# Kernel tuning notes

Measured on AMD Instinct MI355X. Metric: run time of the kernel, lower is better.

The kernel has to match this reference:

```python
import jax, jax.numpy as jnp
import numpy as np

N_NODES = 50000
N_EDGES = 600000
D = 128
EDGE_DIM = 1
N_LAYERS = 2
NEG_SLOPE = 0.2


def setup_inputs() -> dict:
    key = jax.random.key(0)
    ks = jax.random.split(key, 8)
    x = jax.random.normal(ks[0], (N_NODES, D), dtype=jnp.float32)
    edge_index = jax.random.randint(ks[1], (2, N_EDGES), 0, N_NODES, dtype=jnp.int64)
    edge_attr = jax.random.normal(ks[2], (N_EDGES, EDGE_DIM), dtype=jnp.float32)
    s = 1.0 / np.sqrt(D)
    Wl = jax.random.normal(ks[3], (N_LAYERS, D, D), dtype=jnp.float32) * s   # lin_l weights
    Wr = jax.random.normal(ks[4], (N_LAYERS, D, D), dtype=jnp.float32) * s   # lin_r weights
    We = jax.random.normal(ks[5], (N_LAYERS, EDGE_DIM, D), dtype=jnp.float32) * s  # lin_edge
    att = jax.random.normal(ks[6], (N_LAYERS, D), dtype=jnp.float32) * s     # attention vector (heads=1)
    bias = jnp.zeros((N_LAYERS, D), dtype=jnp.float32)
    return {"x": x, "edge_index": edge_index, "edge_attr": edge_attr,
            "Wl": Wl, "Wr": Wr, "We": We, "att": att, "bias": bias}


def _gatv2_layer(x, src, dst, edge_attr, Wl, Wr, We, att, bias):
    # GATv2Conv, heads=1, add_self_loops=False, share_weights=False.
    xl = x @ Wl                                   # [N, D] (source transform)
    xr = x @ Wr                                   # [N, D] (target transform)
    m = xl[src] + xr[dst] + edge_attr @ We        # [E, D]
    m = jax.nn.leaky_relu(m, NEG_SLOPE)
    logits = m @ att                              # [E]
    # segment softmax over incoming edges of each dst node
    mx = jax.ops.segment_max(logits, dst, num_segments=N_NODES)  # [N]
    ex = jnp.exp(logits - mx[dst])                # [E]
    denom = jax.ops.segment_sum(ex, dst, num_segments=N_NODES)   # [N]
    alpha = ex / jnp.maximum(denom[dst], 1e-16)   # [E]
    out = jax.ops.segment_sum(alpha[:, None] * xl[src], dst, num_segments=N_NODES)
    return out + bias


def reference(x, edge_index, edge_attr, Wl, Wr, We, att, bias):
    src, dst = edge_index[0], edge_index[1]
    h = x
    for l in range(N_LAYERS):
        h = _gatv2_layer(h, src, dst, edge_attr, Wl[l], Wr[l], We[l], att[l], bias[l])
        h = jax.nn.relu(h)   # activation; norm=None, dropout=0 (eval) are identity
    return h
```

## Files before the change

kernel.cpp:

```cpp
#include <hip/hip_runtime.h>
#include <hip/hip_fp16.h>

#define N_NODES 50000
#define N_PAD   50048
#define N_EDGES 600000
#define DD 128
#define NEG_SLOPE 0.2f
#define BSHIFT 7
#define NBUCKETS 391
#define MAXB 2048
#define GGRID (N_PAD / 64)

typedef _Float16 h2 __attribute__((ext_vector_type(2)));
typedef _Float16 h8 __attribute__((ext_vector_type(8)));
typedef __attribute__((ext_vector_type(4))) float f32x4;
typedef unsigned long long u64;

__device__ inline h2 bch2(unsigned u) { return __builtin_bit_cast(h2, u); }
__device__ inline unsigned h2u(h2 h) { return __builtin_bit_cast(unsigned, h); }
__device__ inline ushort f2h_bits(float x) {
    return __builtin_bit_cast(ushort, (_Float16)x);
}

#if __has_builtin(__builtin_amdgcn_fdot2)
#define DOT2(a, b, c) __builtin_amdgcn_fdot2((a), (b), (c), false)
#else
#define DOT2(a, b, c) ((c) + (float)(a)[0] * (float)(b)[0] + (float)(a)[1] * (float)(b)[1])
#endif

__global__ void pack_detect(const float* __restrict__ Wl, const float* __restrict__ Wr,
                            ushort* __restrict__ Wp,
                            const int* __restrict__ ei, int* __restrict__ flag,
                            int* __restrict__ bcount) {
    if (blockIdx.x == 256) {
        for (int t = threadIdx.x; t < NBUCKETS; t += 256) bcount[t] = 0;
        if (threadIdx.x == 0) {
            int is64 = 1;
            for (int i = 0; i < 64; ++i) {
                if (ei[2 * i + 1] != 0) { is64 = 0; break; }
            }
            *flag = is64;
        }
        return;
    }
    int idx = blockIdx.x * 256 + threadIdx.x;
    int layer = idx >> 15;
    int which = (idx >> 14) & 1;
    int kk    = (idx >> 12) & 3;
    int c     = (idx >> 9) & 7;
    int lane  = (idx >> 3) & 63;
    int j     = idx & 7;
    int k   = kk * 32 + (lane >> 4) * 8 + j;
    int col = c * 16 + (lane & 15);
    const float* W = which ? Wr : Wl;
    Wp[idx] = f2h_bits(W[(size_t)layer * DD * DD + k * DD + col]);
}

__global__ __launch_bounds__(512) void bin_edges(
    const int* __restrict__ ei, const int* __restrict__ flag,
    const float* __restrict__ ea, int* __restrict__ bcount,
    u64* __restrict__ tmp) {
    __shared__ int lhist[NBUCKETS];
    __shared__ int lbase[NBUCKETS];
    for (int i = threadIdx.x; i < NBUCKETS; i += 512) lhist[i] = 0;
    __syncthreads();
    const bool is64 = (*flag) != 0;
    int base = blockIdx.x * 4096;
    int myb[8], myrank[8];
    u64 mypack[8];
    #pragma unroll
    for (int i = 0; i < 8; ++i) {
        int e = base + i * 512 + threadIdx.x;
        if (e < N_EDGES) {
            int s, d;
            if (is64) {
                const long long* e64 = (const long long*)ei;
                s = (int)e64[e];
                d = (int)e64[N_EDGES + e];
            } else {
                s = ei[e];
                d = ei[N_EDGES + e];
            }
            unsigned hb = (unsigned)f2h_bits(ea[e]);
            int b = d >> BSHIFT;
            myb[i] = b;
            mypack[i] = ((u64)(unsigned)(d & 127) << 32) | ((u64)hb << 16) | (unsigned)s;
            myrank[i] = atomicAdd(&lhist[b], 1);
        } else myb[i] = -1;
    }
    __syncthreads();
    for (int i = threadIdx.x; i < NBUCKETS; i += 512) {
        int c = lhist[i];
        lbase[i] = c ? atomicAdd(&bcount[i], c) : 0;
    }
    __syncthreads();
    #pragma unroll
    for (int i = 0; i < 8; ++i)
        if (myb[i] >= 0) {
            int rel = lbase[myb[i]] + myrank[i];
            if (rel < MAXB)
                tmp[(size_t)myb[i] * MAXB + rel] = mypack[i];
        }
}

__global__ __launch_bounds__(256) void scatter_gemm(
    const u64* __restrict__ tmp, const int* __restrict__ bcount,
    unsigned* __restrict__ se_csr, int* __restrict__ row_start,
    const float* __restrict__ xf, const ushort* __restrict__ Wp,
    ushort* __restrict__ xl, ushort* __restrict__ xr) {
    __shared__ ushort wlds[32768];
    int tid = threadIdx.x;

    if (blockIdx.x < NBUCKETS) {
        int* bscan = (int*)wlds;
        int* lcnt  = (int*)wlds + 512;
        int* lscan = (int*)wlds + 640;
        int* lcur  = (int*)wlds + 768;
        {
            int v = 0;
            if (tid < NBUCKETS) { v = bcount[tid]; if (v > MAXB) v = MAXB; }
            bscan[tid] = v;
            int v2 = 0;
            if (tid + 256 < NBUCKETS) { v2 = bcount[tid + 256]; if (v2 > MAXB) v2 = MAXB; }
            bscan[tid + 256] = v2;
        }
        __syncthreads();
        #pragma unroll
        for (int off = 1; off < 512; off <<= 1) {
            int t0 = (tid >= off) ? bscan[tid - off] : 0;
            int t1 = (tid + 256 >= off) ? bscan[tid + 256 - off] : 0;
            __syncthreads();
            bscan[tid] += t0;
            bscan[tid + 256] += t1;
            __syncthreads();
        }
        int b = blockIdx.x;
        int boff = (b == 0) ? 0 : bscan[b - 1];
        if (b == 0 && tid == 0) row_start[N_NODES] = bscan[NBUCKETS - 1];

        if (tid < 128) lcnt[tid] = 0;
        __syncthreads();
        int n_e = bcount[b]; if (n_e > MAXB) n_e = MAXB;
        const u64* tb = tmp + (size_t)b * MAXB;
        for (int e = tid; e < n_e; e += 256)
            atomicAdd(&lcnt[(int)(tb[e] >> 32)], 1);
        __syncthreads();
        if (tid < 128) lscan[tid] = lcnt[tid];
        __syncthreads();
        #pragma unroll
        for (int off = 1; off < 128; off <<= 1) {
            int t = 0;
            if (tid < 128 && tid >= off) t = lscan[tid - off];
            __syncthreads();
            if (tid < 128) lscan[tid] += t;
            __syncthreads();
        }
        int nb = b << BSHIFT;
        if (tid < 128) {
            int start = boff + lscan[tid] - lcnt[tid];
            lcur[tid] = start;
            if (nb + tid < N_NODES) row_start[nb + tid] = start;
        }
        __syncthreads();
        for (int e = tid; e < n_e; e += 256) {
            u64 w = tb[e];
            int pos = atomicAdd(&lcur[(int)(w >> 32)], 1);
            se_csr[pos] = (unsigned)w;
        }
        return;
    }

    int bid = blockIdx.x - NBUCKETS;
    #pragma unroll
    for (int i = 0; i < 16; ++i) {
        int idx = i * 256 + tid;
        ((uint4*)wlds)[idx] = ((const uint4*)Wp)[idx];
    }
    int wave = tid >> 6, lane = tid & 63;
    int arow = bid * 64 + wave * 16 + (lane & 15);
    int kbase = (lane >> 4) * 8;
    f32x4 accl[8], accr[8];
    #pragma unroll
    for (int c = 0; c < 8; ++c) {
        accl[c] = (f32x4){0.f, 0.f, 0.f, 0.f};
        accr[c] = (f32x4){0.f, 0.f, 0.f, 0.f};
    }
    __syncthreads();
    #pragma unroll
    for (int kk = 0; kk < 4; ++kk) {
        h8 a;
        if (arow < N_NODES) {
            const float* xp = xf + (size_t)arow * DD + kk * 32 + kbase;
            float4 u0 = *(const float4*)xp;
            float4 u1 = *(const float4*)(xp + 4);
            a[0] = (_Float16)u0.x; a[1] = (_Float16)u0.y;
            a[2] = (_Float16)u0.z; a[3] = (_Float16)u0.w;
            a[4] = (_Float16)u1.x; a[5] = (_Float16)u1.y;
            a[6] = (_Float16)u1.z; a[7] = (_Float16)u1.w;
        } else {
            #pragma unroll
            for (int i = 0; i < 8; ++i) a[i] = (_Float16)0.f;
        }
        #pragma unroll
        for (int c = 0; c < 8; ++c) {
            h8 bl = *(const h8*)&wlds[((kk * 8 + c) * 64 + lane) * 8];
            h8 br = *(const h8*)&wlds[16384 + ((kk * 8 + c) * 64 + lane) * 8];
            accl[c] = __builtin_amdgcn_mfma_f32_16x16x32_f16(a, bl, accl[c], 0, 0, 0);
            accr[c] = __builtin_amdgcn_mfma_f32_16x16x32_f16(a, br, accr[c], 0, 0, 0);
        }
    }
    ushort* tile = wlds;
    int drow = wave * 16 + ((lane >> 4) << 2);
    int dcol = lane & 15;
    #pragma unroll
    for (int half = 0; half < 2; ++half) {
        const f32x4* acc = half ? accr : accl;
        ushort* out = half ? xr : xl;
        __syncthreads();
        #pragma unroll
        for (int c = 0; c < 8; ++c)
            #pragma unroll
            for (int r = 0; r < 4; ++r)
                tile[(drow + r) * 136 + c * 16 + dcol] = f2h_bits(acc[c][r]);
        __syncthreads();
        #pragma unroll
        for (int it = 0; it < 8; ++it) {
            int i = it * 256 + tid;
            int row = i >> 5, cc = (i & 31) * 4;
            int gr = bid * 64 + row;
            if (gr < N_NODES)
                *(ushort4*)&out[(size_t)gr * DD + cc] = *(const ushort4*)&tile[row * 136 + cc];
        }
    }
}

__global__ __launch_bounds__(256) void gemm_mfma(
    const ushort* __restrict__ h, const ushort* __restrict__ Wp,
    ushort* __restrict__ xl, ushort* __restrict__ xr) {
    __shared__ ushort wlds[32768];
    #pragma unroll
    for (int i = 0; i < 16; ++i) {
        int idx = i * 256 + threadIdx.x;
        ((uint4*)wlds)[idx] = ((const uint4*)Wp)[idx];
    }
    int wave = threadIdx.x >> 6, lane = threadIdx.x & 63;
    int arow = blockIdx.x * 64 + wave * 16 + (lane & 15);
    int kbase = (lane >> 4) * 8;
    f32x4 accl[8], accr[8];
    #pragma unroll
    for (int c = 0; c < 8; ++c) {
        accl[c] = (f32x4){0.f, 0.f, 0.f, 0.f};
        accr[c] = (f32x4){0.f, 0.f, 0.f, 0.f};
    }
    __syncthreads();
    #pragma unroll
    for (int kk = 0; kk < 4; ++kk) {
        h8 a = *(const h8*)&h[(size_t)arow * DD + kk * 32 + kbase];
        #pragma unroll
        for (int c = 0; c < 8; ++c) {
            h8 bl = *(const h8*)&wlds[((kk * 8 + c) * 64 + lane) * 8];
            h8 br = *(const h8*)&wlds[16384 + ((kk * 8 + c) * 64 + lane) * 8];
            accl[c] = __builtin_amdgcn_mfma_f32_16x16x32_f16(a, bl, accl[c], 0, 0, 0);
            accr[c] = __builtin_amdgcn_mfma_f32_16x16x32_f16(a, br, accr[c], 0, 0, 0);
        }
    }
    ushort* tile = wlds;
    int drow = wave * 16 + ((lane >> 4) << 2);
    int dcol = lane & 15;
    #pragma unroll
    for (int half = 0; half < 2; ++half) {
        const f32x4* acc = half ? accr : accl;
        ushort* out = half ? xr : xl;
        __syncthreads();
        #pragma unroll
        for (int c = 0; c < 8; ++c)
            #pragma unroll
            for (int r = 0; r < 4; ++r)
                tile[(drow + r) * 136 + c * 16 + dcol] = f2h_bits(acc[c][r]);
        __syncthreads();
        #pragma unroll
        for (int it = 0; it < 8; ++it) {
            int i = it * 256 + threadIdx.x;
            int row = i >> 5, cc = (i & 31) * 4;
            int gr = blockIdx.x * 64 + row;
            if (gr < N_NODES)
                *(ushort4*)&out[(size_t)gr * DD + cc] = *(const ushort4*)&tile[row * 136 + cc];
        }
    }
}

template<bool OUT_F16>
__global__ __launch_bounds__(256, 8) void fused_node_f16(
    const ushort* __restrict__ xl, const ushort* __restrict__ xr,
    const float* __restrict__ We, const float* __restrict__ att,
    const int* __restrict__ row_start, const unsigned* __restrict__ se_csr,
    const float* __restrict__ bias, void* __restrict__ outp) {
    int wave = threadIdx.x >> 6;
    int lane = threadIdx.x & 63;
    int n = blockIdx.x * 4 + wave;
    if (n >= N_NODES) return;
    int g  = lane >> 4;
    int cb = (lane & 15) * 8;

    uint4 xrv = *(const uint4*)&xr[(size_t)n * DD + cb];
    h2 xr2[4] = {bch2(xrv.x), bch2(xrv.y), bch2(xrv.z), bch2(xrv.w)};
    float4 wf0 = *(const float4*)&We[cb], wf1 = *(const float4*)&We[cb + 4];
    float4 af0 = *(const float4*)&att[cb], af1 = *(const float4*)&att[cb + 4];
    h2 We2[4] = {{(_Float16)wf0.x, (_Float16)wf0.y}, {(_Float16)wf0.z, (_Float16)wf0.w},
                 {(_Float16)wf1.x, (_Float16)wf1.y}, {(_Float16)wf1.z, (_Float16)wf1.w}};
    h2 at2[4] = {{(_Float16)af0.x, (_Float16)af0.y}, {(_Float16)af0.z, (_Float16)af0.w},
                 {(_Float16)af1.x, (_Float16)af1.y}, {(_Float16)af1.z, (_Float16)af1.w}};
    const h2 ns2 = {(_Float16)NEG_SLOPE, (_Float16)NEG_SLOPE};

    int beg = row_start[n], end = row_start[n + 1];
    h2 acc2[4];
    #pragma unroll
    for (int k = 0; k < 4; ++k) acc2[k] = (h2){(_Float16)0.f, (_Float16)0.f};
    float denom = 0.f;

    for (int j = beg; j < end; j += 16) {
        unsigned w[4]; bool vl[4]; uint4 xv[4];
        #pragma unroll
        for (int q = 0; q < 4; ++q) {
            int e = j + 4 * q + g;
            vl[q] = e < end;
            w[q] = se_csr[vl[q] ? e : (end - 1)];
        }
        #pragma unroll
        for (int q = 0; q < 4; ++q)
            xv[q] = *(const uint4*)&xl[(size_t)(w[q] & 0xffffu) * DD + cb];
        h2 xq[4][4];
        float part[4];
        #pragma unroll
        for (int q = 0; q < 4; ++q) {
            xq[q][0] = bch2(xv[q].x); xq[q][1] = bch2(xv[q].y);
            xq[q][2] = bch2(xv[q].z); xq[q][3] = bch2(xv[q].w);
            h2 a2 = bch2((w[q] >> 16) * 0x10001u);
            float pd = 0.f;
            #pragma unroll
            for (int k = 0; k < 4; ++k) {
                h2 m = __builtin_elementwise_fma(a2, We2[k], xq[q][k] + xr2[k]);
                m = __builtin_elementwise_max(m, m * ns2);
                pd = DOT2(m, at2[k], pd);
            }
            part[q] = pd;
        }
        #pragma unroll
        for (int o = 1; o < 16; o <<= 1) {
            #pragma unroll
            for (int q = 0; q < 4; ++q) part[q] += __shfl_xor(part[q], o, 64);
        }
        #pragma unroll
        for (int q = 0; q < 4; ++q) {
            float p = vl[q] ? __expf(part[q]) : 0.f;
            denom += p;
            _Float16 ph = (_Float16)p;
            h2 p2 = {ph, ph};
            #pragma unroll
            for (int k = 0; k < 4; ++k)
                acc2[k] = __builtin_elementwise_fma(p2, xq[q][k], acc2[k]);
        }
    }

    #pragma unroll
    for (int o = 16; o < 64; o <<= 1) {
        #pragma unroll
        for (int k = 0; k < 4; ++k) {
            int t = __shfl_xor(__builtin_bit_cast(int, acc2[k]), o, 64);
            acc2[k] += __builtin_bit_cast(h2, t);
        }
        denom += __shfl_xor(denom, o, 64);
    }

    if (g == 0) {
        float inv = 1.0f / fmaxf(denom, 1e-16f);
        float o_[8];
        #pragma unroll
        for (int k = 0; k < 4; ++k) {
            o_[2 * k]     = fmaxf(fmaf((float)acc2[k][0], inv, bias[cb + 2 * k]), 0.f);
            o_[2 * k + 1] = fmaxf(fmaf((float)acc2[k][1], inv, bias[cb + 2 * k + 1]), 0.f);
        }
        if (OUT_F16) {
            uint4 o4;
            o4.x = h2u((h2){(_Float16)o_[0], (_Float16)o_[1]});
            o4.y = h2u((h2){(_Float16)o_[2], (_Float16)o_[3]});
            o4.z = h2u((h2){(_Float16)o_[4], (_Float16)o_[5]});
            o4.w = h2u((h2){(_Float16)o_[6], (_Float16)o_[7]});
            *(uint4*)((ushort*)outp + (size_t)n * DD + cb) = o4;
        } else {
            float* op = (float*)outp + (size_t)n * DD + cb;
            *(float4*)op       = *(float4*)&o_[0];
            *(float4*)(op + 4) = *(float4*)&o_[4];
        }
    }
}

extern "C" void kernel_launch(void* const* d_in, const int* in_sizes, int n_in,
                              void* d_out, int out_size, void* d_ws, size_t ws_size,
                              hipStream_t stream) {
    const float* x    = (const float*)d_in[0];
    const int*   ei   = (const int*)d_in[1];
    const float* ea   = (const float*)d_in[2];
    const float* Wl   = (const float*)d_in[3];
    const float* Wr   = (const float*)d_in[4];
    const float* We   = (const float*)d_in[5];
    const float* att  = (const float*)d_in[6];
    const float* bias = (const float*)d_in[7];

    char* wsb = (char*)d_ws;
    size_t off = 0;
    auto alloc = [&](size_t bytes) { void* r = (void*)(wsb + off); off += (bytes + 15) & ~15ull; return r; };
    ushort* h_f16    = (ushort*)alloc((size_t)N_PAD * DD * 2);
    ushort* xl_f16   = (ushort*)alloc((size_t)N_NODES * DD * 2);
    ushort* xr_f16   = (ushort*)alloc((size_t)N_NODES * DD * 2);
    ushort* Wp       = (ushort*)alloc(65536 * 2);
    u64*    tmp      = (u64*)alloc((size_t)NBUCKETS * MAXB * 8);
    unsigned* se_csr = (unsigned*)alloc((size_t)N_EDGES * 4);
    int*    row_st   = (int*)alloc((N_NODES + 1) * 4);
    int*    bcount   = (int*)alloc(NBUCKETS * 4);
    int*    flag     = (int*)alloc(4);

    pack_detect<<<257, 256, 0, stream>>>(Wl, Wr, Wp, ei, flag, bcount);

    bin_edges<<<(N_EDGES + 4095) / 4096, 512, 0, stream>>>(ei, flag, ea, bcount, tmp);

    scatter_gemm<<<NBUCKETS + GGRID, 256, 0, stream>>>(
        tmp, bcount, se_csr, row_st, x, Wp, xl_f16, xr_f16);

    fused_node_f16<true><<<(N_NODES + 3) / 4, 256, 0, stream>>>(
        xl_f16, xr_f16, We, att, row_st, se_csr, bias, (void*)h_f16);

    gemm_mfma<<<GGRID, 256, 0, stream>>>(h_f16, Wp + 32768, xl_f16, xr_f16);
    fused_node_f16<false><<<(N_NODES + 3) / 4, 256, 0, stream>>>(
        xl_f16, xr_f16, We + DD, att + DD, row_st, se_csr, bias + DD, d_out);
}
```

Baseline: 119.9 us.

## Split layer-1 aggregation by node halves and overlap layer-2 GEMM with second half

Layer-1 node aggregation is split at a node boundary. A combined kernel runs the layer-2 GEMM for the first half of the rows alongside the aggregation of the second half, and a trailing GEMM then covers the remaining rows. Separate xl2/xr2 buffers are added so the GEMM does not overwrite xl/xr while aggregation still reads them. The intent is to fill idle compute units during the tail of the gather-bound aggregation and to hide the GEMM. It costs an extra launch, extra workspace, and a combined kernel whose GEMM blocks read weights from global memory instead of LDS.

New measurement: 145.8 us. 21.6% more time.

```diff
diff --git a/kernel.cpp b/kernel.cpp
--- a/kernel.cpp
+++ b/kernel.cpp
@@ -10,6 +10,10 @@
 #define NBUCKETS 391
 #define MAXB 2048
 #define GGRID (N_PAD / 64)
+#define NSPLIT 25024
+#define GH (NSPLIT / 64)
+#define FA (NSPLIT / 4)
+#define FB ((N_NODES - NSPLIT + 3) / 4)
 
 typedef _Float16 h2 __attribute__((ext_vector_type(2)));
 typedef _Float16 h8 __attribute__((ext_vector_type(8)));
@@ -234,71 +238,13 @@
     }
 }
 
-__global__ __launch_bounds__(256) void gemm_mfma(
-    const ushort* __restrict__ h, const ushort* __restrict__ Wp,
-    ushort* __restrict__ xl, ushort* __restrict__ xr) {
-    __shared__ ushort wlds[32768];
-    #pragma unroll
-    for (int i = 0; i < 16; ++i) {
-        int idx = i * 256 + threadIdx.x;
-        ((uint4*)wlds)[idx] = ((const uint4*)Wp)[idx];
-    }
-    int wave = threadIdx.x >> 6, lane = threadIdx.x & 63;
-    int arow = blockIdx.x * 64 + wave * 16 + (lane & 15);
-    int kbase = (lane >> 4) * 8;
-    f32x4 accl[8], accr[8];
-    #pragma unroll
-    for (int c = 0; c < 8; ++c) {
-        accl[c] = (f32x4){0.f, 0.f, 0.f, 0.f};
-        accr[c] = (f32x4){0.f, 0.f, 0.f, 0.f};
-    }
-    __syncthreads();
-    #pragma unroll
-    for (int kk = 0; kk < 4; ++kk) {
-        h8 a = *(const h8*)&h[(size_t)arow * DD + kk * 32 + kbase];
-        #pragma unroll
-        for (int c = 0; c < 8; ++c) {
-            h8 bl = *(const h8*)&wlds[((kk * 8 + c) * 64 + lane) * 8];
-            h8 br = *(const h8*)&wlds[16384 + ((kk * 8 + c) * 64 + lane) * 8];
-            accl[c] = __builtin_amdgcn_mfma_f32_16x16x32_f16(a, bl, accl[c], 0, 0, 0);
-            accr[c] = __builtin_amdgcn_mfma_f32_16x16x32_f16(a, br, accr[c], 0, 0, 0);
-        }
-    }
-    ushort* tile = wlds;
-    int drow = wave * 16 + ((lane >> 4) << 2);
-    int dcol = lane & 15;
-    #pragma unroll
-    for (int half = 0; half < 2; ++half) {
-        const f32x4* acc = half ? accr : accl;
-        ushort* out = half ? xr : xl;
-        __syncthreads();
-        #pragma unroll
-        for (int c = 0; c < 8; ++c)
-            #pragma unroll
-            for (int r = 0; r < 4; ++r)
-                tile[(drow + r) * 136 + c * 16 + dcol] = f2h_bits(acc[c][r]);
-        __syncthreads();
-        #pragma unroll
-        for (int it = 0; it < 8; ++it) {
-            int i = it * 256 + threadIdx.x;
-            int row = i >> 5, cc = (i & 31) * 4;
-            int gr = blockIdx.x * 64 + row;
-            if (gr < N_NODES)
-                *(ushort4*)&out[(size_t)gr * DD + cc] = *(const ushort4*)&tile[row * 136 + cc];
-        }
-    }
-}
-
 template<bool OUT_F16>
-__global__ __launch_bounds__(256, 8) void fused_node_f16(
+__device__ __forceinline__ void fused_body(
+    int n, int lane,
     const ushort* __restrict__ xl, const ushort* __restrict__ xr,
     const float* __restrict__ We, const float* __restrict__ att,
     const int* __restrict__ row_start, const unsigned* __restrict__ se_csr,
     const float* __restrict__ bias, void* __restrict__ outp) {
-    int wave = threadIdx.x >> 6;
-    int lane = threadIdx.x & 63;
-    int n = blockIdx.x * 4 + wave;
-    if (n >= N_NODES) return;
     int g  = lane >> 4;
     int cb = (lane & 15) * 8;
 
@@ -395,6 +341,135 @@
     }
 }
 
+template<bool OUT_F16>
+__global__ __launch_bounds__(256, 8) void fused_node_f16(
+    const ushort* __restrict__ xl, const ushort* __restrict__ xr,
+    const float* __restrict__ We, const float* __restrict__ att,
+    const int* __restrict__ row_start, const unsigned* __restrict__ se_csr,
+    const float* __restrict__ bias, void* __restrict__ outp,
+    int nbase, int nlim) {
+    int wave = threadIdx.x >> 6, lane = threadIdx.x & 63;
+    int n = nbase + blockIdx.x * 4 + wave;
+    if (n >= nlim) return;
+    fused_body<OUT_F16>(n, lane, xl, xr, We, att, row_start, se_csr, bias, outp);
+}
+
+__global__ __launch_bounds__(256) void fused0b_gemm1a(
+    const ushort* __restrict__ xl, const ushort* __restrict__ xr,
+    const float* __restrict__ We, const float* __restrict__ att,
+    const int* __restrict__ row_start, const unsigned* __restrict__ se_csr,
+    const float* __restrict__ bias, ushort* __restrict__ h_out,
+    const ushort* __restrict__ hsrc, const ushort* __restrict__ Wp1,
+    ushort* __restrict__ xl2, ushort* __restrict__ xr2) {
+    __shared__ ushort tile[64 * 136];
+    int tid = threadIdx.x, wave = tid >> 6, lane = tid & 63;
+
+    if (blockIdx.x >= GH) {
+        int n = NSPLIT + (int)(blockIdx.x - GH) * 4 + wave;
+        if (n < N_NODES)
+            fused_body<true>(n, lane, xl, xr, We, att, row_start, se_csr, bias, h_out);
+        return;
+    }
+
+    int arow = blockIdx.x * 64 + wave * 16 + (lane & 15);
+    int kbase = (lane >> 4) * 8;
+    f32x4 accl[8], accr[8];
+    #pragma unroll
+    for (int c = 0; c < 8; ++c) {
+        accl[c] = (f32x4){0.f, 0.f, 0.f, 0.f};
+        accr[c] = (f32x4){0.f, 0.f, 0.f, 0.f};
+    }
+    h8 a[4];
+    #pragma unroll
+    for (int kk = 0; kk < 4; ++kk)
+        a[kk] = *(const h8*)&hsrc[(size_t)arow * DD + kk * 32 + kbase];
+    #pragma unroll
+    for (int kk = 0; kk < 4; ++kk)
+        #pragma unroll
+        for (int c = 0; c < 8; ++c) {
+            h8 bl = *(const h8*)&Wp1[((size_t)(kk * 8 + c) * 64 + lane) * 8];
+            h8 br = *(const h8*)&Wp1[16384 + ((size_t)(kk * 8 + c) * 64 + lane) * 8];
+            accl[c] = __builtin_amdgcn_mfma_f32_16x16x32_f16(a[kk], bl, accl[c], 0, 0, 0);
+            accr[c] = __builtin_amdgcn_mfma_f32_16x16x32_f16(a[kk], br, accr[c], 0, 0, 0);
+        }
+    int drow = wave * 16 + ((lane >> 4) << 2);
+    int dcol = lane & 15;
+    #pragma unroll
+    for (int half = 0; half < 2; ++half) {
+        const f32x4* acc = half ? accr : accl;
+        ushort* out = half ? xr2 : xl2;
+        __syncthreads();
+        #pragma unroll
+        for (int c = 0; c < 8; ++c)
+            #pragma unroll
+            for (int r = 0; r < 4; ++r)
+                tile[(drow + r) * 136 + c * 16 + dcol] = f2h_bits(acc[c][r]);
+        __syncthreads();
+        #pragma unroll
+        for (int it = 0; it < 8; ++it) {
+            int i = it * 256 + tid;
+            int row = i >> 5, cc = (i & 31) * 4;
+            int gr = blockIdx.x * 64 + row;
+            *(ushort4*)&out[(size_t)gr * DD + cc] = *(const ushort4*)&tile[row * 136 + cc];
+        }
+    }
+}
+
+__global__ __launch_bounds__(256) void gemm_mfma(
+    const ushort* __restrict__ h, const ushort* __restrict__ Wp,
+    ushort* __restrict__ xl, ushort* __restrict__ xr, int rbase) {
+    __shared__ ushort wlds[32768];
+    #pragma unroll
+    for (int i = 0; i < 16; ++i) {
+        int idx = i * 256 + threadIdx.x;
+        ((uint4*)wlds)[idx] = ((const uint4*)Wp)[idx];
+    }
+    int wave = threadIdx.x >> 6, lane = threadIdx.x & 63;
+    int arow = rbase + blockIdx.x * 64 + wave * 16 + (lane & 15);
+    int kbase = (lane >> 4) * 8;
+    f32x4 accl[8], accr[8];
+    #pragma unroll
+    for (int c = 0; c < 8; ++c) {
+        accl[c] = (f32x4){0.f, 0.f, 0.f, 0.f};
+        accr[c] = (f32x4){0.f, 0.f, 0.f, 0.f};
+    }
+    __syncthreads();
+    #pragma unroll
+    for (int kk = 0; kk < 4; ++kk) {
+        h8 a = *(const h8*)&h[(size_t)arow * DD + kk * 32 + kbase];
+        #pragma unroll
+        for (int c = 0; c < 8; ++c) {
+            h8 bl = *(const h8*)&wlds[((kk * 8 + c) * 64 + lane) * 8];
+            h8 br = *(const h8*)&wlds[16384 + ((kk * 8 + c) * 64 + lane) * 8];
+            accl[c] = __builtin_amdgcn_mfma_f32_16x16x32_f16(a, bl, accl[c], 0, 0, 0);
+            accr[c] = __builtin_amdgcn_mfma_f32_16x16x32_f16(a, br, accr[c], 0, 0, 0);
+        }
+    }
+    ushort* tile = wlds;
+    int drow = wave * 16 + ((lane >> 4) << 2);
+    int dcol = lane & 15;
+    #pragma unroll
+    for (int half = 0; half < 2; ++half) {
+        const f32x4* acc = half ? accr : accl;
+        ushort* out = half ? xr : xl;
+        __syncthreads();
+        #pragma unroll
+        for (int c = 0; c < 8; ++c)
+            #pragma unroll
+            for (int r = 0; r < 4; ++r)
+                tile[(drow + r) * 136 + c * 16 + dcol] = f2h_bits(acc[c][r]);
+        __syncthreads();
+        #pragma unroll
+        for (int it = 0; it < 8; ++it) {
+            int i = it * 256 + threadIdx.x;
+            int row = i >> 5, cc = (i & 31) * 4;
+            int gr = rbase + blockIdx.x * 64 + row;
+            if (gr < N_NODES)
+                *(ushort4*)&out[(size_t)gr * DD + cc] = *(const ushort4*)&tile[row * 136 + cc];
+        }
+    }
+}
+
 extern "C" void kernel_launch(void* const* d_in, const int* in_sizes, int n_in,
                               void* d_out, int out_size, void* d_ws, size_t ws_size,
                               hipStream_t stream) {
@@ -413,6 +488,8 @@
     ushort* h_f16    = (ushort*)alloc((size_t)N_PAD * DD * 2);
     ushort* xl_f16   = (ushort*)alloc((size_t)N_NODES * DD * 2);
     ushort* xr_f16   = (ushort*)alloc((size_t)N_NODES * DD * 2);
+    ushort* xl2_f16  = (ushort*)alloc((size_t)N_NODES * DD * 2);
+    ushort* xr2_f16  = (ushort*)alloc((size_t)N_NODES * DD * 2);
     ushort* Wp       = (ushort*)alloc(65536 * 2);
     u64*    tmp      = (u64*)alloc((size_t)NBUCKETS * MAXB * 8);
     unsigned* se_csr = (unsigned*)alloc((size_t)N_EDGES * 4);
@@ -427,10 +504,16 @@
     scatter_gemm<<<NBUCKETS + GGRID, 256, 0, stream>>>(
         tmp, bcount, se_csr, row_st, x, Wp, xl_f16, xr_f16);
 
-    fused_node_f16<true><<<(N_NODES + 3) / 4, 256, 0, stream>>>(
-        xl_f16, xr_f16, We, att, row_st, se_csr, bias, (void*)h_f16);
-
-    gemm_mfma<<<GGRID, 256, 0, stream>>>(h_f16, Wp + 32768, xl_f16, xr_f16);
+    fused_node_f16<true><<<FA, 256, 0, stream>>>(
+        xl_f16, xr_f16, We, att, row_st, se_csr, bias, (void*)h_f16, 0, NSPLIT);
+
+    fused0b_gemm1a<<<GH + FB, 256, 0, stream>>>(
+        xl_f16, xr_f16, We, att, row_st, se_csr, bias, h_f16,
+        h_f16, Wp + 32768, xl2_f16, xr2_f16);
+
+    gemm_mfma<<<(N_PAD - NSPLIT) / 64, 256, 0, stream>>>(
+        h_f16, Wp + 32768, xl2_f16, xr2_f16, NSPLIT);
+
     fused_node_f16<false><<<(N_NODES + 3) / 4, 256, 0, stream>>>(
-        xl_f16, xr_f16, We + DD, att + DD, row_st, se_csr, bias + DD, d_out);
-}
+        xl2_f16, xr2_f16, We + DD, att + DD, row_st, se_csr, bias + DD, d_out, 0, N_NODES);
+}
```
